# Kernel tuning notes

Hardware: AMD Instinct MI355X
Metric: run time of the kernel (lower is better)

Reference implementation:

```python
import jax, jax.numpy as jnp
import numpy as np

EMBED = 1024
HIDDEN = 4 * EMBED
EPS = 1e-5

def _layer_norm(x, g, b):
    mu = jnp.mean(x, axis=-1, keepdims=True)
    var = jnp.mean((x - mu) ** 2, axis=-1, keepdims=True)
    return (x - mu) * jax.lax.rsqrt(var + EPS) * g + b

def setup_inputs() -> dict:
    key = jax.random.key(0)
    ks = jax.random.split(key, 8)
    s = 1.0 / np.sqrt(EMBED)
    inp = {
        "x": jax.random.normal(ks[0], (4, 2048, EMBED), dtype=jnp.float32),
        "Wq": jax.random.normal(ks[1], (EMBED, EMBED), dtype=jnp.float32) * s,
        "bq": jnp.zeros((EMBED,), jnp.float32),
        "Wk": jax.random.normal(ks[2], (EMBED, EMBED), dtype=jnp.float32) * s,
        "bk": jnp.zeros((EMBED,), jnp.float32),
        "Wv": jax.random.normal(ks[3], (EMBED, EMBED), dtype=jnp.float32) * s,
        "bv": jnp.zeros((EMBED,), jnp.float32),
        "W1": jax.random.normal(ks[4], (EMBED, HIDDEN), dtype=jnp.float32) * s,
        "b1": jnp.zeros((HIDDEN,), jnp.float32),
        "W2": jax.random.normal(ks[5], (HIDDEN, EMBED), dtype=jnp.float32) * (1.0 / np.sqrt(HIDDEN)),
        "b2": jnp.zeros((EMBED,), jnp.float32),
        "g1": jnp.ones((EMBED,), jnp.float32),
        "be1": jnp.zeros((EMBED,), jnp.float32),
        "g2": jnp.ones((EMBED,), jnp.float32),
        "be2": jnp.zeros((EMBED,), jnp.float32),
    }
    return inp

def reference(x, Wq, bq, Wk, bk, Wv, bv, W1, b1, W2, b2, g1, be1, g2, be2):
    # pre-norm attention
    h = _layer_norm(x, g1, be1)
    Q = h @ Wq + bq  # [B,S,D]
    K = h @ Wk + bk
    V = h @ Wv + bv
    scale = 1.0 / jnp.sqrt(jnp.asarray(EMBED, x.dtype))
    scores = jnp.einsum('bqd,bkd->bqk', Q, K) * scale  # [B,S,S]
    weights = jax.nn.softmax(scores, axis=-1)
    attn = jnp.einsum('bqk,bkd->bqd', weights, V)
    x = x + attn
    # pre-norm MLP
    h2 = _layer_norm(x, g2, be2)
    ff = jax.nn.relu(h2 @ W1 + b1) @ W2 + b2
    return x + ff
```

## Files before the change

kernel.cpp:

```cpp
#include <hip/hip_runtime.h>

#define EMBED 1024
#define HID   4096
#define NB    4
#define SEQ   2048

typedef __attribute__((ext_vector_type(8)))  __bf16 bf16x8;
typedef __attribute__((ext_vector_type(4)))  float  f32x4;
typedef __attribute__((ext_vector_type(4)))  int    i32x4;
typedef unsigned short u16;

__device__ __forceinline__ u16 f2bf(float f) {
  unsigned u = __float_as_uint(f);
  u += 0x7FFFu + ((u >> 16) & 1u);
  return (u16)(u >> 16);
}
__device__ __forceinline__ float bf2f(u16 u) {
  return __uint_as_float(((unsigned)u) << 16);
}

typedef const __attribute__((address_space(1))) unsigned int* gas_t;
typedef __attribute__((address_space(3))) unsigned int* las_t;
__device__ __forceinline__ void gld16(const void* g, void* l) {
  __builtin_amdgcn_global_load_lds((gas_t)g, (las_t)l, 16, 0, 0);
}

#define RD16(p)       __builtin_bit_cast(bf16x8, *(const i32x4*)(p))
#define MFMA16(a,b,c) __builtin_amdgcn_mfma_f32_16x16x32_bf16(a, b, c, 0, 0, 0)
#define SCHED0()      __builtin_amdgcn_sched_barrier(0)
#define BARR()        __builtin_amdgcn_s_barrier()
#define LGKM(n)       asm volatile("s_waitcnt lgkmcnt(" #n ")" ::: "memory")
#define VMW(n)        asm volatile("s_waitcnt vmcnt(" #n ")" ::: "memory")

template<int EPI>
__global__ __launch_bounds__(512, 2) void gemm256v3(
    const u16* __restrict__ A, int lda, long long astr,
    const u16* __restrict__ B, int ldb, long long bstr,
    void* __restrict__ C, int ldc, long long cstr,
    const float* __restrict__ bias,
    float scale, int Kdim)
{
  __shared__ char lds[131072];

  const int tid  = threadIdx.x;
  const int lane = tid & 63;
  const int w    = tid >> 6;
  const int wr   = w >> 2, wc = w & 3;
  const int l15  = lane & 15, l4 = lane >> 4;

  const int gx   = gridDim.x;
  const int nwg  = gx * gridDim.y;
  const int orig = blockIdx.y * gx + blockIdx.x;
  const int t    = ((nwg & 7) == 0) ? ((orig & 7) * (nwg >> 3) + (orig >> 3)) : orig;
  const int bx   = t % gx, by = t / gx;

  const u16* Ab = A + (size_t)blockIdx.z * astr + (size_t)by * 256 * lda;
  const u16* Bb = B + (size_t)blockIdx.z * bstr + (size_t)bx * 256 * ldb;

  const int    srow = tid >> 3;
  const size_t sa   = (size_t)srow * lda + (size_t)(((tid & 7) ^ (srow & 7)) * 8);
  const size_t sb   = (size_t)srow * ldb + (size_t)(((tid & 7) ^ (srow & 7)) * 8);
  const int    ldst = tid * 16;

  auto stA = [&](int buf, int q, int kk) {
    gld16(Ab + (size_t)(q * 64) * lda + kk + sa, lds + buf * 65536 + q * 8192 + ldst);
  };
  auto stB = [&](int buf, int i, int kk) {
    gld16(Bb + (size_t)(i * 64) * ldb + kk + sb, lds + buf * 65536 + 32768 + i * 8192 + ldst);
  };

  const int arow = (wr * 128 + l15) * 128;
  const int brow = 32768 + (wc * 64 + l15) * 128;
  const int cp0  = ((0 + l4) ^ (l15 & 7)) * 16;
  const int cp1  = ((4 + l4) ^ (l15 & 7)) * 16;

  f32x4 acc[8][4] = {};
  const int NT = Kdim >> 6;

  stB(0, 0, 0); stB(0, 1, 0); stB(0, 2, 0); stB(0, 3, 0);
  stA(0, 0, 0); stA(0, 1, 0); stA(0, 2, 0); stA(0, 3, 0);

  for (int T = 0; T < NT; ++T) {
    const char* LB = lds + (T & 1) * 65536;
    VMW(0);
    SCHED0();
    BARR();
    SCHED0();

    if (T + 1 < NT) {
      const int b = (T & 1) ^ 1, kk = (T + 1) * 64;
      stB(b, 0, kk); stB(b, 1, kk); stB(b, 2, kk); stB(b, 3, kk);
      stA(b, 0, kk); stA(b, 1, kk); stA(b, 2, kk); stA(b, 3, kk);
    }

    bf16x8 b0 = RD16(LB + brow + 0 * 2048 + cp0);
    bf16x8 b1 = RD16(LB + brow + 1 * 2048 + cp0);
    bf16x8 b2 = RD16(LB + brow + 2 * 2048 + cp0);
    bf16x8 b3 = RD16(LB + brow + 3 * 2048 + cp0);
    bf16x8 b4 = RD16(LB + brow + 0 * 2048 + cp1);
    bf16x8 b5 = RD16(LB + brow + 1 * 2048 + cp1);
    bf16x8 b6 = RD16(LB + brow + 2 * 2048 + cp1);
    bf16x8 b7 = RD16(LB + brow + 3 * 2048 + cp1);

#define AQ(MP, x0, x1, x2, x3) \
    bf16x8 x0 = RD16(LB + arow + (MP) * 4096 + cp0); \
    bf16x8 x1 = RD16(LB + arow + (MP) * 4096 + cp1); \
    bf16x8 x2 = RD16(LB + arow + (MP) * 4096 + 2048 + cp0); \
    bf16x8 x3 = RD16(LB + arow + (MP) * 4096 + 2048 + cp1);

#define MQ(MP, x0, x1, x2, x3) \
    acc[2*(MP)  ][0] = MFMA16(x0, b0, acc[2*(MP)  ][0]); \
    acc[2*(MP)  ][1] = MFMA16(x0, b1, acc[2*(MP)  ][1]); \
    acc[2*(MP)  ][2] = MFMA16(x0, b2, acc[2*(MP)  ][2]); \
    acc[2*(MP)  ][3] = MFMA16(x0, b3, acc[2*(MP)  ][3]); \
    acc[2*(MP)+1][0] = MFMA16(x2, b0, acc[2*(MP)+1][0]); \
    acc[2*(MP)+1][1] = MFMA16(x2, b1, acc[2*(MP)+1][1]); \
    acc[2*(MP)+1][2] = MFMA16(x2, b2, acc[2*(MP)+1][2]); \
    acc[2*(MP)+1][3] = MFMA16(x2, b3, acc[2*(MP)+1][3]); \
    acc[2*(MP)  ][0] = MFMA16(x1, b4, acc[2*(MP)  ][0]); \
    acc[2*(MP)  ][1] = MFMA16(x1, b5, acc[2*(MP)  ][1]); \
    acc[2*(MP)  ][2] = MFMA16(x1, b6, acc[2*(MP)  ][2]); \
    acc[2*(MP)  ][3] = MFMA16(x1, b7, acc[2*(MP)  ][3]); \
    acc[2*(MP)+1][0] = MFMA16(x3, b4, acc[2*(MP)+1][0]); \
    acc[2*(MP)+1][1] = MFMA16(x3, b5, acc[2*(MP)+1][1]); \
    acc[2*(MP)+1][2] = MFMA16(x3, b6, acc[2*(MP)+1][2]); \
    acc[2*(MP)+1][3] = MFMA16(x3, b7, acc[2*(MP)+1][3]);

    AQ(0, a00, a01, a02, a03)
    AQ(1, a10, a11, a12, a13)
    MQ(0, a00, a01, a02, a03)
    AQ(2, a20, a21, a22, a23)
    MQ(1, a10, a11, a12, a13)
    AQ(3, a30, a31, a32, a33)
    MQ(2, a20, a21, a22, a23)
    MQ(3, a30, a31, a32, a33)
#undef AQ
#undef MQ
  }

  const int bm0 = by * 256 + wr * 128;
  const int bn0 = bx * 256 + wc * 64;
  u16* Ch = (u16*)C;
  #pragma unroll
  for (int mi = 0; mi < 8; ++mi) {
    #pragma unroll
    for (int ni = 0; ni < 4; ++ni) {
      const int col = bn0 + ni * 16 + l15;
      const int r0  = bm0 + mi * 16 + l4 * 4;
      float bv = 0.f;
      if (EPI == 0 || EPI == 3) bv = bias[col];
      #pragma unroll
      for (int r = 0; r < 4; ++r) {
        const size_t idx = (size_t)blockIdx.z * cstr + (size_t)(r0 + r) * ldc + col;
        const float v = acc[mi][ni][r];
        if      (EPI == 0) Ch[idx] = f2bf(v + bv);
        else if (EPI == 3) Ch[idx] = f2bf(fmaxf(v + bv, 0.f));
        else if (EPI == 6) Ch[idx] = f2bf(v * scale);
      }
    }
  }
}

template<int EPI>
__global__ __launch_bounds__(512, 2) void gemm8p(
    const u16* __restrict__ A, int lda, long long astr,
    const u16* __restrict__ B, int ldb, long long bstr,
    void* __restrict__ C, int ldc, long long cstr,
    const float* __restrict__ bias,
    const float* __restrict__ add,
    float scale, int Kdim)
{
  __shared__ i32x4 lds4[9216];
  const int SLOT = 49152;

  const int tid  = threadIdx.x;
  const int lane = tid & 63;
  const int w    = tid >> 6;
  const int wr   = w >> 1, wc = w & 1;
  const int l15  = lane & 15, l4 = lane >> 4;

  const int gx   = gridDim.x;
  const int nwg  = gx * gridDim.y;
  const int orig = blockIdx.y * gx + blockIdx.x;
  const int t    = ((nwg & 7) == 0) ? ((orig & 7) * (nwg >> 3) + (orig >> 3)) : orig;
  const int bx   = t % gx, by = t / gx;

  const u16* Ab = A + (size_t)blockIdx.z * astr + (size_t)by * 256 * lda;
  const u16* Bb = B + (size_t)blockIdx.z * bstr + (size_t)bx * 128 * ldb;

  size_t gaoff[4], gboff[2];
  #pragma unroll
  for (int i = 0; i < 4; ++i) {
    const int idx = i * 512 + tid, row = idx >> 3, gc = (idx & 7) ^ (row & 7);
    gaoff[i] = (size_t)row * lda + gc * 8;
  }
  #pragma unroll
  for (int j = 0; j < 2; ++j) {
    const int idx = j * 512 + tid, row = idx >> 3, gc = (idx & 7) ^ (row & 7);
    gboff[j] = (size_t)row * ldb + gc * 8;
  }

  int aoff[4], boff[4], cp16[2];
  #pragma unroll
  for (int m = 0; m < 4; ++m) aoff[m] = (wr * 64 + m * 16 + l15) * 128;
  #pragma unroll
  for (int n = 0; n < 4; ++n) boff[n] = 32768 + (wc * 64 + n * 16 + l15) * 128;
  cp16[0] = ((0 + l4) ^ (l15 & 7)) * 16;
  cp16[1] = ((4 + l4) ^ (l15 & 7)) * 16;

  f32x4 acc[4][4] = {};
  const int NT = Kdim >> 6;
  char* lbase = (char*)lds4;

  {
    char* s0 = lbase;
    char* s1 = lbase + SLOT;
    #pragma unroll
    for (int i = 0; i < 4; ++i) gld16(Ab + gaoff[i],      s0 + (i * 512 + w * 64) * 16);
    #pragma unroll
    for (int j = 0; j < 2; ++j) gld16(Bb + gboff[j],      s0 + 32768 + (j * 512 + w * 64) * 16);
    #pragma unroll
    for (int i = 0; i < 4; ++i) gld16(Ab + gaoff[i] + 64, s1 + (i * 512 + w * 64) * 16);
    #pragma unroll
    for (int j = 0; j < 2; ++j) gld16(Bb + gboff[j] + 64, s1 + 32768 + (j * 512 + w * 64) * 16);
  }

  int s = 0;
  for (int T = 0; T < NT; ++T) {
    const bool st  = (T + 2 < NT);
    const size_t kk = (size_t)(T + 2) * 64;
    const char* rA = lbase + s * SLOT;
    char* wS = lbase + ((s + 2 >= 3) ? (s - 1) : (s + 2)) * SLOT;

    if (T == NT - 1) VMW(0);
    else             VMW(6);
    BARR();
    SCHED0();

    bf16x8 b0, b1, b2, b3, a0, a1;

    b0 = RD16(rA + boff[0] + cp16[0]);
    b1 = RD16(rA + boff[1] + cp16[0]);
    b2 = RD16(rA + boff[2] + cp16[0]);
    b3 = RD16(rA + boff[3] + cp16[0]);
    a0 = RD16(rA + aoff[0] + cp16[0]);
    a1 = RD16(rA + aoff[1] + cp16[0]);
    if (st) {
      gld16(Ab + gaoff[0] + kk, wS + (0 * 512 + w * 64) * 16);
      gld16(Ab + gaoff[1] + kk, wS + (1 * 512 + w * 64) * 16);
    }
    BARR();
    LGKM(0);
    SCHED0();
    __builtin_amdgcn_s_setprio(1);
    acc[0][0] = MFMA16(a0, b0, acc[0][0]);
    acc[0][1] = MFMA16(a0, b1, acc[0][1]);
    acc[0][2] = MFMA16(a0, b2, acc[0][2]);
    acc[0][3] = MFMA16(a0, b3, acc[0][3]);
    acc[1][0] = MFMA16(a1, b0, acc[1][0]);
    acc[1][1] = MFMA16(a1, b1, acc[1][1]);
    acc[1][2] = MFMA16(a1, b2, acc[1][2]);
    acc[1][3] = MFMA16(a1, b3, acc[1][3]);
    __builtin_amdgcn_s_setprio(0);

    a0 = RD16(rA + aoff[2] + cp16[0]);
    a1 = RD16(rA + aoff[3] + cp16[0]);
    if (st) {
      gld16(Ab + gaoff[2] + kk, wS + (2 * 512 + w * 64) * 16);
      gld16(Ab + gaoff[3] + kk, wS + (3 * 512 + w * 64) * 16);
    }
    BARR();
    LGKM(0);
    SCHED0();
    __builtin_amdgcn_s_setprio(1);
    acc[2][0] = MFMA16(a0, b0, acc[2][0]);
    acc[2][1] = MFMA16(a0, b1, acc[2][1]);
    acc[2][2] = MFMA16(a0, b2, acc[2][2]);
    acc[2][3] = MFMA16(a0, b3, acc[2][3]);
    acc[3][0] = MFMA16(a1, b0, acc[3][0]);
    acc[3][1] = MFMA16(a1, b1, acc[3][1]);
    acc[3][2] = MFMA16(a1, b2, acc[3][2]);
    acc[3][3] = MFMA16(a1, b3, acc[3][3]);
    __builtin_amdgcn_s_setprio(0);

    b0 = RD16(rA + boff[0] + cp16[1]);
    b1 = RD16(rA + boff[1] + cp16[1]);
    b2 = RD16(rA + boff[2] + cp16[1]);
    b3 = RD16(rA + boff[3] + cp16[1]);
    a0 = RD16(rA + aoff[0] + cp16[1]);
    a1 = RD16(rA + aoff[1] + cp16[1]);
    if (st) {
      gld16(Bb + gboff[0] + kk, wS + 32768 + (0 * 512 + w * 64) * 16);
    }
    BARR();
    LGKM(0);
    SCHED0();
    __builtin_amdgcn_s_setprio(1);
    acc[0][0] = MFMA16(a0, b0, acc[0][0]);
    acc[0][1] = MFMA16(a0, b1, acc[0][1]);
    acc[0][2] = MFMA16(a0, b2, acc[0][2]);
    acc[0][3] = MFMA16(a0, b3, acc[0][3]);
    acc[1][0] = MFMA16(a1, b0, acc[1][0]);
    acc[1][1] = MFMA16(a1, b1, acc[1][1]);
    acc[1][2] = MFMA16(a1, b2, acc[1][2]);
    acc[1][3] = MFMA16(a1, b3, acc[1][3]);
    __builtin_amdgcn_s_setprio(0);

    a0 = RD16(rA + aoff[2] + cp16[1]);
    a1 = RD16(rA + aoff[3] + cp16[1]);
    if (st) {
      gld16(Bb + gboff[1] + kk, wS + 32768 + (1 * 512 + w * 64) * 16);
    }
    BARR();
    LGKM(0);
    SCHED0();
    __builtin_amdgcn_s_setprio(1);
    acc[2][0] = MFMA16(a0, b0, acc[2][0]);
    acc[2][1] = MFMA16(a0, b1, acc[2][1]);
    acc[2][2] = MFMA16(a0, b2, acc[2][2]);
    acc[2][3] = MFMA16(a0, b3, acc[2][3]);
    acc[3][0] = MFMA16(a1, b0, acc[3][0]);
    acc[3][1] = MFMA16(a1, b1, acc[3][1]);
    acc[3][2] = MFMA16(a1, b2, acc[3][2]);
    acc[3][3] = MFMA16(a1, b3, acc[3][3]);
    __builtin_amdgcn_s_setprio(0);

    s = (s + 1 == 3) ? 0 : s + 1;
  }

  const int bm0 = by * 256 + wr * 64;
  const int bn0 = bx * 128 + wc * 64;
  float* Cf = (float*)C;
  u16*   Ch = (u16*)C;
  #pragma unroll
  for (int mi = 0; mi < 4; ++mi) {
    #pragma unroll
    for (int ni = 0; ni < 4; ++ni) {
      const int col = bn0 + ni * 16 + l15;
      const int r0  = bm0 + mi * 16 + l4 * 4;
      float bv = 0.f;
      if (EPI == 0 || EPI == 4) bv = bias[col];
      #pragma unroll
      for (int r = 0; r < 4; ++r) {
        const size_t idx = (size_t)blockIdx.z * cstr + (size_t)(r0 + r) * ldc + col;
        const float v = acc[mi][ni][r];
        if      (EPI == 0) Ch[idx] = f2bf(v + bv);
        else if (EPI == 1) Cf[idx] = v * scale;
        else if (EPI == 2) Cf[idx] = v + add[idx];
        else if (EPI == 4) Cf[idx] = v + bv + add[idx];
        else if (EPI == 5) Ch[idx] = f2bf(v + bias[r0 + r]);
        else if (EPI == 6) Ch[idx] = f2bf(v * scale);
      }
    }
  }
}

__global__ __launch_bounds__(256) void ln_kernel(
    const float* __restrict__ x, const float* __restrict__ g,
    const float* __restrict__ be, u16* __restrict__ out)
{
  const int row = blockIdx.x;
  const int tid = threadIdx.x;
  const float4 v = ((const float4*)(x + (size_t)row * EMBED))[tid];
  float s  = v.x + v.y + v.z + v.w;
  float s2 = v.x * v.x + v.y * v.y + v.z * v.z + v.w * v.w;
  #pragma unroll
  for (int m = 1; m < 64; m <<= 1) { s += __shfl_xor(s, m); s2 += __shfl_xor(s2, m); }
  __shared__ float ls[4], ls2[4];
  const int w = tid >> 6;
  if ((tid & 63) == 0) { ls[w] = s; ls2[w] = s2; }
  __syncthreads();
  s  = ls[0] + ls[1] + ls[2] + ls[3];
  s2 = ls2[0] + ls2[1] + ls2[2] + ls2[3];
  const float mu   = s * (1.f / EMBED);
  const float var  = s2 * (1.f / EMBED) - mu * mu;
  const float rstd = rsqrtf(var + 1e-5f);
  const float4 gv = ((const float4*)g)[tid];
  const float4 bv = ((const float4*)be)[tid];
  ushort4 o;
  o.x = f2bf((v.x - mu) * rstd * gv.x + bv.x);
  o.y = f2bf((v.y - mu) * rstd * gv.y + bv.y);
  o.z = f2bf((v.z - mu) * rstd * gv.z + bv.z);
  o.w = f2bf((v.w - mu) * rstd * gv.w + bv.w);
  ((ushort4*)(out + (size_t)row * EMBED))[tid] = o;
}

__global__ __launch_bounds__(256) void softmax_bf16(
    const u16* __restrict__ S, u16* __restrict__ P)
{
  const int tid = threadIdx.x;
  const size_t base = ((size_t)blockIdx.y * SEQ + blockIdx.x) * SEQ;
  const ushort4* src = (const ushort4*)(S + base);
  const ushort4 ua = src[tid];
  const ushort4 ub = src[tid + 256];
  float a0 = bf2f(ua.x), a1 = bf2f(ua.y), a2 = bf2f(ua.z), a3 = bf2f(ua.w);
  float b0 = bf2f(ub.x), b1 = bf2f(ub.y), b2 = bf2f(ub.z), b3 = bf2f(ub.w);
  float m = fmaxf(fmaxf(fmaxf(a0, a1), fmaxf(a2, a3)),
                  fmaxf(fmaxf(b0, b1), fmaxf(b2, b3)));
  #pragma unroll
  for (int msk = 1; msk < 64; msk <<= 1) m = fmaxf(m, __shfl_xor(m, msk));
  __shared__ float red[8];
  const int w = tid >> 6;
  if ((tid & 63) == 0) red[w] = m;
  __syncthreads();
  m = fmaxf(fmaxf(red[0], red[1]), fmaxf(red[2], red[3]));
  a0 = __expf(a0 - m); a1 = __expf(a1 - m); a2 = __expf(a2 - m); a3 = __expf(a3 - m);
  b0 = __expf(b0 - m); b1 = __expf(b1 - m); b2 = __expf(b2 - m); b3 = __expf(b3 - m);
  float s = a0 + a1 + a2 + a3 + b0 + b1 + b2 + b3;
  #pragma unroll
  for (int msk = 1; msk < 64; msk <<= 1) s += __shfl_xor(s, msk);
  if ((tid & 63) == 0) red[4 + w] = s;
  __syncthreads();
  s = red[4] + red[5] + red[6] + red[7];
  const float inv = 1.0f / s;
  ushort4 oa, ob;
  oa.x = f2bf(a0 * inv); oa.y = f2bf(a1 * inv); oa.z = f2bf(a2 * inv); oa.w = f2bf(a3 * inv);
  ob.x = f2bf(b0 * inv); ob.y = f2bf(b1 * inv); ob.z = f2bf(b2 * inv); ob.w = f2bf(b3 * inv);
  ushort4* dst = (ushort4*)(P + base);
  dst[tid]       = oa;
  dst[tid + 256] = ob;
}

__global__ void transpose_cast3(const float* __restrict__ W0,
                                const float* __restrict__ W1_,
                                const float* __restrict__ W2_,
                                u16* __restrict__ Wt)
{
  __shared__ float t[32][33];
  const int z = blockIdx.z;
  const float* W = (z == 0) ? W0 : (z == 1) ? W1_ : W2_;
  u16* dst = Wt + (size_t)z * EMBED * EMBED;
  const int tx = threadIdx.x, ty = threadIdx.y;
  const int n0 = blockIdx.x * 32, k0 = blockIdx.y * 32;
  #pragma unroll
  for (int i = 0; i < 4; ++i)
    t[ty + i * 8][tx] = W[(size_t)(k0 + ty + i * 8) * EMBED + n0 + tx];
  __syncthreads();
  #pragma unroll
  for (int i = 0; i < 4; ++i)
    dst[(size_t)(n0 + ty + i * 8) * EMBED + k0 + tx] = f2bf(t[tx][ty + i * 8]);
}

__global__ void transpose_cast_f32(const float* __restrict__ W, u16* __restrict__ Wt,
                                   int K, int N)
{
  __shared__ float t[32][33];
  const int tx = threadIdx.x, ty = threadIdx.y;
  const int n0 = blockIdx.x * 32, k0 = blockIdx.y * 32;
  #pragma unroll
  for (int i = 0; i < 4; ++i)
    t[ty + i * 8][tx] = W[(size_t)(k0 + ty + i * 8) * N + n0 + tx];
  __syncthreads();
  #pragma unroll
  for (int i = 0; i < 4; ++i)
    Wt[(size_t)(n0 + ty + i * 8) * K + k0 + tx] = f2bf(t[tx][ty + i * 8]);
}

__global__ void concat_bias2(const float* __restrict__ a, const float* __restrict__ b,
                             float* __restrict__ o)
{
  const int i = blockIdx.x * 1024 + threadIdx.x;
  o[i] = (i < 1024) ? a[i] : b[i - 1024];
}

extern "C" void kernel_launch(void* const* d_in, const int* in_sizes, int n_in,
                              void* d_out, int out_size, void* d_ws, size_t ws_size,
                              hipStream_t stream)
{
  const float* x   = (const float*)d_in[0];
  const float* Wq  = (const float*)d_in[1];
  const float* bq  = (const float*)d_in[2];
  const float* Wk  = (const float*)d_in[3];
  const float* bk  = (const float*)d_in[4];
  const float* Wv  = (const float*)d_in[5];
  const float* bv  = (const float*)d_in[6];
  const float* W1  = (const float*)d_in[7];
  const float* b1  = (const float*)d_in[8];
  const float* W2  = (const float*)d_in[9];
  const float* b2  = (const float*)d_in[10];
  const float* g1  = (const float*)d_in[11];
  const float* be1 = (const float*)d_in[12];
  const float* g2  = (const float*)d_in[13];
  const float* be2 = (const float*)d_in[14];
  float* out = (float*)d_out;

  const size_t RD = (size_t)NB * SEQ * EMBED;

  char* base = (char*)d_ws;
  size_t o = 0;
  auto alloc = [&](size_t bytes) -> void* {
    o = (o + 255) & ~(size_t)255;
    void* p = base + o;
    o += bytes;
    return p;
  };

  u16*   wqkv3T = (u16*)alloc((size_t)3 * EMBED * EMBED * 2);
  u16*   w1T    = (u16*)alloc((size_t)HID * EMBED * 2);
  u16*   w2T    = (u16*)alloc((size_t)EMBED * HID * 2);
  float* bqk    = (float*)alloc(2048 * 4);
  u16*   h      = (u16*)alloc(RD * 2);
  u16*   QKb    = (u16*)alloc(RD * 2 * 2);
  u16*   Vt     = (u16*)alloc(RD * 2);
  float* x2     = (float*)alloc(RD * 4);

  const size_t need_batched = o + (size_t)NB * SEQ * SEQ * 4 + 1024;
  const int NZ = (ws_size >= need_batched) ? NB : 1;
  u16* Sb16 = (u16*)alloc((size_t)NZ * SEQ * SEQ * 2);
  u16* Pb   = (u16*)alloc((size_t)NZ * SEQ * SEQ * 2);
  u16* ff   = (NZ == NB) ? Sb16
                         : (u16*)alloc((size_t)NB * SEQ * HID * 2);

  const u16* wqkT = wqkv3T;
  const u16* wvT  = wqkv3T + (size_t)2 * EMBED * EMBED;

  const dim3 blk(512);
  const dim3 tblk(32, 8);

  transpose_cast3<<<dim3(32, 32, 3), tblk, 0, stream>>>(Wq, Wk, Wv, wqkv3T);
  transpose_cast_f32<<<dim3(HID / 32, EMBED / 32), tblk, 0, stream>>>(W1, w1T, EMBED, HID);
  transpose_cast_f32<<<dim3(EMBED / 32, HID / 32), tblk, 0, stream>>>(W2, w2T, HID, EMBED);
  concat_bias2<<<dim3(2), dim3(1024), 0, stream>>>(bq, bk, bqk);

  ln_kernel<<<dim3(NB * SEQ), dim3(256), 0, stream>>>(x, g1, be1, h);

  gemm256v3<0><<<dim3(2048 / 256, NB * SEQ / 256, 1), blk, 0, stream>>>(
      h, EMBED, 0LL, wqkT, EMBED, 0LL, QKb, 2048, 0LL, bqk, 1.f, EMBED);

  gemm8p<5><<<dim3(SEQ / 128, EMBED / 256, NB), blk, 0, stream>>>(
      wvT, EMBED, 0LL, h, EMBED, (long long)SEQ * EMBED,
      Vt, SEQ, (long long)EMBED * SEQ, bv, nullptr, 1.f, EMBED);

  for (int b = 0; b < NB; b += NZ) {
    const u16* Qp  = QKb + (size_t)b * SEQ * 2048;
    const u16* Kp  = Qp + 1024;
    const u16* Vtp = Vt + (size_t)b * EMBED * SEQ;
    float* x2p     = x2 + (size_t)b * SEQ * EMBED;
    const float* xp = x + (size_t)b * SEQ * EMBED;
    gemm256v3<6><<<dim3(SEQ / 256, SEQ / 256, NZ), blk, 0, stream>>>(
        Qp, 2048, (long long)SEQ * 2048, Kp, 2048, (long long)SEQ * 2048,
        Sb16, SEQ, (long long)SEQ * SEQ, nullptr, 0.03125f, EMBED);
    softmax_bf16<<<dim3(SEQ, NZ), dim3(256), 0, stream>>>(Sb16, Pb);
    gemm8p<2><<<dim3(EMBED / 128, SEQ / 256, NZ), blk, 0, stream>>>(
        Pb, SEQ, (long long)SEQ * SEQ, Vtp, SEQ, (long long)EMBED * SEQ,
        x2p, EMBED, (long long)SEQ * EMBED, nullptr, xp, 1.f, SEQ);
  }

  ln_kernel<<<dim3(NB * SEQ), dim3(256), 0, stream>>>(x2, g2, be2, h);

  gemm256v3<3><<<dim3(HID / 256, NB * SEQ / 256, 1), blk, 0, stream>>>(
      h, EMBED, 0LL, w1T, EMBED, 0LL, ff, HID, 0LL, b1, 1.f, EMBED);
  gemm8p<4><<<dim3(EMBED / 128, NB * SEQ / 256, 1), blk, 0, stream>>>(
      ff, HID, 0LL, w2T, HID, 0LL, out, EMBED, 0LL, b2, x2, 1.f, HID);
}
```

Baseline: 321.9 us.

## Replace 3-stage interleaved GEMM pipeline with double-buffer; store residual in bf16

The 256x128 GEMM drops its three-slot LDS ring with interleaved partial loads and per-chunk barriers. It now uses a two-slot double buffer: it waits on all vector loads, stages the next tile, reads all fragments and issues 32 MFMAs in one go. Separately, the attention residual x2 is now stored as bf16 instead of fp32, with a new bf16 LayerNorm kernel and a bf16 add in the final GEMM epilogue, which halves traffic for that tensor. This trades pipeline depth and overlap for simplicity, and lowers residual precision in a way that may affect accuracy.

```diff
diff --git a/kernel.cpp b/kernel.cpp
--- a/kernel.cpp
+++ b/kernel.cpp
@@ -29,7 +29,6 @@
 #define MFMA16(a,b,c) __builtin_amdgcn_mfma_f32_16x16x32_bf16(a, b, c, 0, 0, 0)
 #define SCHED0()      __builtin_amdgcn_sched_barrier(0)
 #define BARR()        __builtin_amdgcn_s_barrier()
-#define LGKM(n)       asm volatile("s_waitcnt lgkmcnt(" #n ")" ::: "memory")
 #define VMW(n)        asm volatile("s_waitcnt vmcnt(" #n ")" ::: "memory")
 
 template<int EPI>
@@ -162,16 +161,15 @@
 }
 
 template<int EPI>
-__global__ __launch_bounds__(512, 2) void gemm8p(
+__global__ __launch_bounds__(512, 2) void gemm128v3(
     const u16* __restrict__ A, int lda, long long astr,
     const u16* __restrict__ B, int ldb, long long bstr,
     void* __restrict__ C, int ldc, long long cstr,
     const float* __restrict__ bias,
-    const float* __restrict__ add,
+    const void* __restrict__ add,
     float scale, int Kdim)
 {
-  __shared__ i32x4 lds4[9216];
-  const int SLOT = 49152;
+  __shared__ char lds[98304];
 
   const int tid  = threadIdx.x;
   const int lane = tid & 63;
@@ -200,138 +198,92 @@
     gboff[j] = (size_t)row * ldb + gc * 8;
   }
 
-  int aoff[4], boff[4], cp16[2];
+  auto stage = [&](char* SB, int kk) {
+    #pragma unroll
+    for (int i = 0; i < 4; ++i) gld16(Ab + gaoff[i] + kk, SB + (i * 512 + w * 64) * 16);
+    #pragma unroll
+    for (int j = 0; j < 2; ++j) gld16(Bb + gboff[j] + kk, SB + 32768 + (j * 512 + w * 64) * 16);
+  };
+
+  int aoff[4], boff[4];
   #pragma unroll
   for (int m = 0; m < 4; ++m) aoff[m] = (wr * 64 + m * 16 + l15) * 128;
   #pragma unroll
   for (int n = 0; n < 4; ++n) boff[n] = 32768 + (wc * 64 + n * 16 + l15) * 128;
-  cp16[0] = ((0 + l4) ^ (l15 & 7)) * 16;
-  cp16[1] = ((4 + l4) ^ (l15 & 7)) * 16;
+  const int cp0 = ((0 + l4) ^ (l15 & 7)) * 16;
+  const int cp1 = ((4 + l4) ^ (l15 & 7)) * 16;
 
   f32x4 acc[4][4] = {};
   const int NT = Kdim >> 6;
-  char* lbase = (char*)lds4;
-
-  {
-    char* s0 = lbase;
-    char* s1 = lbase + SLOT;
-    #pragma unroll
-    for (int i = 0; i < 4; ++i) gld16(Ab + gaoff[i],      s0 + (i * 512 + w * 64) * 16);
-    #pragma unroll
-    for (int j = 0; j < 2; ++j) gld16(Bb + gboff[j],      s0 + 32768 + (j * 512 + w * 64) * 16);
-    #pragma unroll
-    for (int i = 0; i < 4; ++i) gld16(Ab + gaoff[i] + 64, s1 + (i * 512 + w * 64) * 16);
-    #pragma unroll
-    for (int j = 0; j < 2; ++j) gld16(Bb + gboff[j] + 64, s1 + 32768 + (j * 512 + w * 64) * 16);
-  }
-
-  int s = 0;
+
+  stage(lds, 0);
+
   for (int T = 0; T < NT; ++T) {
-    const bool st  = (T + 2 < NT);
-    const size_t kk = (size_t)(T + 2) * 64;
-    const char* rA = lbase + s * SLOT;
-    char* wS = lbase + ((s + 2 >= 3) ? (s - 1) : (s + 2)) * SLOT;
-
-    if (T == NT - 1) VMW(0);
-    else             VMW(6);
+    const char* LB = lds + (T & 1) * 49152;
+    VMW(0);
+    SCHED0();
     BARR();
     SCHED0();
 
-    bf16x8 b0, b1, b2, b3, a0, a1;
-
-    b0 = RD16(rA + boff[0] + cp16[0]);
-    b1 = RD16(rA + boff[1] + cp16[0]);
-    b2 = RD16(rA + boff[2] + cp16[0]);
-    b3 = RD16(rA + boff[3] + cp16[0]);
-    a0 = RD16(rA + aoff[0] + cp16[0]);
-    a1 = RD16(rA + aoff[1] + cp16[0]);
-    if (st) {
-      gld16(Ab + gaoff[0] + kk, wS + (0 * 512 + w * 64) * 16);
-      gld16(Ab + gaoff[1] + kk, wS + (1 * 512 + w * 64) * 16);
-    }
-    BARR();
-    LGKM(0);
-    SCHED0();
-    __builtin_amdgcn_s_setprio(1);
-    acc[0][0] = MFMA16(a0, b0, acc[0][0]);
-    acc[0][1] = MFMA16(a0, b1, acc[0][1]);
-    acc[0][2] = MFMA16(a0, b2, acc[0][2]);
-    acc[0][3] = MFMA16(a0, b3, acc[0][3]);
-    acc[1][0] = MFMA16(a1, b0, acc[1][0]);
-    acc[1][1] = MFMA16(a1, b1, acc[1][1]);
-    acc[1][2] = MFMA16(a1, b2, acc[1][2]);
-    acc[1][3] = MFMA16(a1, b3, acc[1][3]);
-    __builtin_amdgcn_s_setprio(0);
-
-    a0 = RD16(rA + aoff[2] + cp16[0]);
-    a1 = RD16(rA + aoff[3] + cp16[0]);
-    if (st) {
-      gld16(Ab + gaoff[2] + kk, wS + (2 * 512 + w * 64) * 16);
-      gld16(Ab + gaoff[3] + kk, wS + (3 * 512 + w * 64) * 16);
-    }
-    BARR();
-    LGKM(0);
-    SCHED0();
-    __builtin_amdgcn_s_setprio(1);
-    acc[2][0] = MFMA16(a0, b0, acc[2][0]);
-    acc[2][1] = MFMA16(a0, b1, acc[2][1]);
-    acc[2][2] = MFMA16(a0, b2, acc[2][2]);
-    acc[2][3] = MFMA16(a0, b3, acc[2][3]);
-    acc[3][0] = MFMA16(a1, b0, acc[3][0]);
-    acc[3][1] = MFMA16(a1, b1, acc[3][1]);
-    acc[3][2] = MFMA16(a1, b2, acc[3][2]);
-    acc[3][3] = MFMA16(a1, b3, acc[3][3]);
-    __builtin_amdgcn_s_setprio(0);
-
-    b0 = RD16(rA + boff[0] + cp16[1]);
-    b1 = RD16(rA + boff[1] + cp16[1]);
-    b2 = RD16(rA + boff[2] + cp16[1]);
-    b3 = RD16(rA + boff[3] + cp16[1]);
-    a0 = RD16(rA + aoff[0] + cp16[1]);
-    a1 = RD16(rA + aoff[1] + cp16[1]);
-    if (st) {
-      gld16(Bb + gboff[0] + kk, wS + 32768 + (0 * 512 + w * 64) * 16);
-    }
-    BARR();
-    LGKM(0);
-    SCHED0();
-    __builtin_amdgcn_s_setprio(1);
-    acc[0][0] = MFMA16(a0, b0, acc[0][0]);
-    acc[0][1] = MFMA16(a0, b1, acc[0][1]);
-    acc[0][2] = MFMA16(a0, b2, acc[0][2]);
-    acc[0][3] = MFMA16(a0, b3, acc[0][3]);
-    acc[1][0] = MFMA16(a1, b0, acc[1][0]);
-    acc[1][1] = MFMA16(a1, b1, acc[1][1]);
-    acc[1][2] = MFMA16(a1, b2, acc[1][2]);
-    acc[1][3] = MFMA16(a1, b3, acc[1][3]);
-    __builtin_amdgcn_s_setprio(0);
-
-    a0 = RD16(rA + aoff[2] + cp16[1]);
-    a1 = RD16(rA + aoff[3] + cp16[1]);
-    if (st) {
-      gld16(Bb + gboff[1] + kk, wS + 32768 + (1 * 512 + w * 64) * 16);
-    }
-    BARR();
-    LGKM(0);
-    SCHED0();
-    __builtin_amdgcn_s_setprio(1);
-    acc[2][0] = MFMA16(a0, b0, acc[2][0]);
-    acc[2][1] = MFMA16(a0, b1, acc[2][1]);
-    acc[2][2] = MFMA16(a0, b2, acc[2][2]);
-    acc[2][3] = MFMA16(a0, b3, acc[2][3]);
-    acc[3][0] = MFMA16(a1, b0, acc[3][0]);
-    acc[3][1] = MFMA16(a1, b1, acc[3][1]);
-    acc[3][2] = MFMA16(a1, b2, acc[3][2]);
-    acc[3][3] = MFMA16(a1, b3, acc[3][3]);
-    __builtin_amdgcn_s_setprio(0);
-
-    s = (s + 1 == 3) ? 0 : s + 1;
+    if (T + 1 < NT) stage(lds + ((T & 1) ^ 1) * 49152, (T + 1) * 64);
+
+    bf16x8 b00 = RD16(LB + boff[0] + cp0);
+    bf16x8 b01 = RD16(LB + boff[1] + cp0);
+    bf16x8 b02 = RD16(LB + boff[2] + cp0);
+    bf16x8 b03 = RD16(LB + boff[3] + cp0);
+    bf16x8 b10 = RD16(LB + boff[0] + cp1);
+    bf16x8 b11 = RD16(LB + boff[1] + cp1);
+    bf16x8 b12 = RD16(LB + boff[2] + cp1);
+    bf16x8 b13 = RD16(LB + boff[3] + cp1);
+    bf16x8 a00 = RD16(LB + aoff[0] + cp0);
+    bf16x8 a10 = RD16(LB + aoff[1] + cp0);
+    bf16x8 a20 = RD16(LB + aoff[2] + cp0);
+    bf16x8 a30 = RD16(LB + aoff[3] + cp0);
+    bf16x8 a01 = RD16(LB + aoff[0] + cp1);
+    bf16x8 a11 = RD16(LB + aoff[1] + cp1);
+    bf16x8 a21 = RD16(LB + aoff[2] + cp1);
+    bf16x8 a31 = RD16(LB + aoff[3] + cp1);
+
+    acc[0][0] = MFMA16(a00, b00, acc[0][0]);
+    acc[0][1] = MFMA16(a00, b01, acc[0][1]);
+    acc[0][2] = MFMA16(a00, b02, acc[0][2]);
+    acc[0][3] = MFMA16(a00, b03, acc[0][3]);
+    acc[1][0] = MFMA16(a10, b00, acc[1][0]);
+    acc[1][1] = MFMA16(a10, b01, acc[1][1]);
+    acc[1][2] = MFMA16(a10, b02, acc[1][2]);
+    acc[1][3] = MFMA16(a10, b03, acc[1][3]);
+    acc[2][0] = MFMA16(a20, b00, acc[2][0]);
+    acc[2][1] = MFMA16(a20, b01, acc[2][1]);
+    acc[2][2] = MFMA16(a20, b02, acc[2][2]);
+    acc[2][3] = MFMA16(a20, b03, acc[2][3]);
+    acc[3][0] = MFMA16(a30, b00, acc[3][0]);
+    acc[3][1] = MFMA16(a30, b01, acc[3][1]);
+    acc[3][2] = MFMA16(a30, b02, acc[3][2]);
+    acc[3][3] = MFMA16(a30, b03, acc[3][3]);
+    acc[0][0] = MFMA16(a01, b10, acc[0][0]);
+    acc[0][1] = MFMA16(a01, b11, acc[0][1]);
+    acc[0][2] = MFMA16(a01, b12, acc[0][2]);
+    acc[0][3] = MFMA16(a01, b13, acc[0][3]);
+    acc[1][0] = MFMA16(a11, b10, acc[1][0]);
+    acc[1][1] = MFMA16(a11, b11, acc[1][1]);
+    acc[1][2] = MFMA16(a11, b12, acc[1][2]);
+    acc[1][3] = MFMA16(a11, b13, acc[1][3]);
+    acc[2][0] = MFMA16(a21, b10, acc[2][0]);
+    acc[2][1] = MFMA16(a21, b11, acc[2][1]);
+    acc[2][2] = MFMA16(a21, b12, acc[2][2]);
+    acc[2][3] = MFMA16(a21, b13, acc[2][3]);
+    acc[3][0] = MFMA16(a31, b10, acc[3][0]);
+    acc[3][1] = MFMA16(a31, b11, acc[3][1]);
+    acc[3][2] = MFMA16(a31, b12, acc[3][2]);
+    acc[3][3] = MFMA16(a31, b13, acc[3][3]);
   }
 
   const int bm0 = by * 256 + wr * 64;
   const int bn0 = bx * 128 + wc * 64;
   float* Cf = (float*)C;
   u16*   Ch = (u16*)C;
+  const float* addf = (const float*)add;
+  const u16*   addh = (const u16*)add;
   #pragma unroll
   for (int mi = 0; mi < 4; ++mi) {
     #pragma unroll
@@ -339,17 +291,14 @@
       const int col = bn0 + ni * 16 + l15;
       const int r0  = bm0 + mi * 16 + l4 * 4;
       float bv = 0.f;
-      if (EPI == 0 || EPI == 4) bv = bias[col];
+      if (EPI == 8) bv = bias[col];
       #pragma unroll
       for (int r = 0; r < 4; ++r) {
         const size_t idx = (size_t)blockIdx.z * cstr + (size_t)(r0 + r) * ldc + col;
         const float v = acc[mi][ni][r];
-        if      (EPI == 0) Ch[idx] = f2bf(v + bv);
-        else if (EPI == 1) Cf[idx] = v * scale;
-        else if (EPI == 2) Cf[idx] = v + add[idx];
-        else if (EPI == 4) Cf[idx] = v + bv + add[idx];
-        else if (EPI == 5) Ch[idx] = f2bf(v + bias[r0 + r]);
-        else if (EPI == 6) Ch[idx] = f2bf(v * scale);
+        if      (EPI == 5) Ch[idx] = f2bf(v + bias[r0 + r]);
+        else if (EPI == 7) Ch[idx] = f2bf(v + addf[idx]);
+        else if (EPI == 8) Cf[idx] = v + bv + bf2f(addh[idx]);
       }
     }
   }
@@ -385,6 +334,37 @@
   ((ushort4*)(out + (size_t)row * EMBED))[tid] = o;
 }
 
+__global__ __launch_bounds__(256) void ln_bf16(
+    const u16* __restrict__ x, const float* __restrict__ g,
+    const float* __restrict__ be, u16* __restrict__ out)
+{
+  const int row = blockIdx.x;
+  const int tid = threadIdx.x;
+  const ushort4 u = ((const ushort4*)(x + (size_t)row * EMBED))[tid];
+  float v0 = bf2f(u.x), v1 = bf2f(u.y), v2 = bf2f(u.z), v3 = bf2f(u.w);
+  float s  = v0 + v1 + v2 + v3;
+  float s2 = v0 * v0 + v1 * v1 + v2 * v2 + v3 * v3;
+  #pragma unroll
+  for (int m = 1; m < 64; m <<= 1) { s += __shfl_xor(s, m); s2 += __shfl_xor(s2, m); }
+  __shared__ float ls[4], ls2[4];
+  const int w = tid >> 6;
+  if ((tid & 63) == 0) { ls[w] = s; ls2[w] = s2; }
+  __syncthreads();
+  s  = ls[0] + ls[1] + ls[2] + ls[3];
+  s2 = ls2[0] + ls2[1] + ls2[2] + ls2[3];
+  const float mu   = s * (1.f / EMBED);
+  const float var  = s2 * (1.f / EMBED) - mu * mu;
+  const float rstd = rsqrtf(var + 1e-5f);
+  const float4 gv = ((const float4*)g)[tid];
+  const float4 bv = ((const float4*)be)[tid];
+  ushort4 o;
+  o.x = f2bf((v0 - mu) * rstd * gv.x + bv.x);
+  o.y = f2bf((v1 - mu) * rstd * gv.y + bv.y);
+  o.z = f2bf((v2 - mu) * rstd * gv.z + bv.z);
+  o.w = f2bf((v3 - mu) * rstd * gv.w + bv.w);
+  ((ushort4*)(out + (size_t)row * EMBED))[tid] = o;
+}
+
 __global__ __launch_bounds__(256) void softmax_bf16(
     const u16* __restrict__ S, u16* __restrict__ P)
 {
@@ -502,7 +482,7 @@
   u16*   h      = (u16*)alloc(RD * 2);
   u16*   QKb    = (u16*)alloc(RD * 2 * 2);
   u16*   Vt     = (u16*)alloc(RD * 2);
-  float* x2     = (float*)alloc(RD * 4);
+  u16*   x2     = (u16*)alloc(RD * 2);
 
   const size_t need_batched = o + (size_t)NB * SEQ * SEQ * 4 + 1024;
   const int NZ = (ws_size >= need_batched) ? NB : 1;
@@ -527,7 +507,7 @@
   gemm256v3<0><<<dim3(2048 / 256, NB * SEQ / 256, 1), blk, 0, stream>>>(
       h, EMBED, 0LL, wqkT, EMBED, 0LL, QKb, 2048, 0LL, bqk, 1.f, EMBED);
 
-  gemm8p<5><<<dim3(SEQ / 128, EMBED / 256, NB), blk, 0, stream>>>(
+  gemm128v3<5><<<dim3(SEQ / 128, EMBED / 256, NB), blk, 0, stream>>>(
       wvT, EMBED, 0LL, h, EMBED, (long long)SEQ * EMBED,
       Vt, SEQ, (long long)EMBED * SEQ, bv, nullptr, 1.f, EMBED);
 
@@ -535,21 +515,21 @@
     const u16* Qp  = QKb + (size_t)b * SEQ * 2048;
     const u16* Kp  = Qp + 1024;
     const u16* Vtp = Vt + (size_t)b * EMBED * SEQ;
-    float* x2p     = x2 + (size_t)b * SEQ * EMBED;
+    u16* x2p       = x2 + (size_t)b * SEQ * EMBED;
     const float* xp = x + (size_t)b * SEQ * EMBED;
     gemm256v3<6><<<dim3(SEQ / 256, SEQ / 256, NZ), blk, 0, stream>>>(
         Qp, 2048, (long long)SEQ * 2048, Kp, 2048, (long long)SEQ * 2048,
         Sb16, SEQ, (long long)SEQ * SEQ, nullptr, 0.03125f, EMBED);
     softmax_bf16<<<dim3(SEQ, NZ), dim3(256), 0, stream>>>(Sb16, Pb);
-    gemm8p<2><<<dim3(EMBED / 128, SEQ / 256, NZ), blk, 0, stream>>>(
+    gemm128v3<7><<<dim3(EMBED / 128, SEQ / 256, NZ), blk, 0, stream>>>(
         Pb, SEQ, (long long)SEQ * SEQ, Vtp, SEQ, (long long)EMBED * SEQ,
         x2p, EMBED, (long long)SEQ * EMBED, nullptr, xp, 1.f, SEQ);
   }
 
-  ln_kernel<<<dim3(NB * SEQ), dim3(256), 0, stream>>>(x2, g2, be2, h);
+  ln_bf16<<<dim3(NB * SEQ), dim3(256), 0, stream>>>(x2, g2, be2, h);
 
   gemm256v3<3><<<dim3(HID / 256, NB * SEQ / 256, 1), blk, 0, stream>>>(
       h, EMBED, 0LL, w1T, EMBED, 0LL, ff, HID, 0LL, b1, 1.f, EMBED);
-  gemm8p<4><<<dim3(EMBED / 128, NB * SEQ / 256, 1), blk, 0, stream>>>(
+  gemm128v3<8><<<dim3(EMBED / 128, NB * SEQ / 256, 1), blk, 0, stream>>>(
       ff, HID, 0LL, w2T, HID, 0LL, out, EMBED, 0LL, b2, x2, 1.f, HID);
 }
```

Measured after the change: 319.5 us. About the same (-0.8%).
